# Performance work log

Hardware: AMD Instinct MI355X
Metric: run time of the kernel (lower is better)

## Reference

```python
import jax, jax.numpy as jnp
import numpy as np

B, S, DIM = 4, 512, 2048
E, INTER = 32, 1024
G, TOPK_G, TOPK = 8, 4, 6
ROUTE_SCALE = 2.5
SHARED_INTER = 2 * INTER  # n_shared_experts * moe_inter_dim


def setup_inputs() -> dict:
    key = jax.random.key(0)
    ks = jax.random.split(key, 8)
    sd = 0.02
    return {
        "x": jax.random.normal(ks[0], (B, S, DIM), jnp.float32),
        "gate_w": jax.random.normal(ks[1], (E, DIM), jnp.float32) * sd,
        "w11": jax.random.normal(ks[2], (E, INTER, DIM), jnp.float32) * sd,  # gate proj (torch Linear weight [out,in])
        "w33": jax.random.normal(ks[3], (E, INTER, DIM), jnp.float32) * sd,  # up proj
        "w22": jax.random.normal(ks[4], (E, DIM, INTER), jnp.float32) * sd,  # down proj
        "sw1": jax.random.normal(ks[5], (SHARED_INTER, DIM), jnp.float32) * sd,
        "sw2": jax.random.normal(ks[6], (DIM, SHARED_INTER), jnp.float32) * sd,
        "sw3": jax.random.normal(ks[7], (SHARED_INTER, DIM), jnp.float32) * sd,
    }


def _gate(xf, gate_w):
    # sigmoid scores, group-limited greedy top-k (bias=None branch)
    scores = jax.nn.sigmoid(xf @ gate_w.T)                      # [T, E]
    gs = scores.reshape(-1, G, E // G)                          # [T, G, E/G]
    group_scores = gs.max(axis=-1)                              # amax since bias is None
    _, gidx = jax.lax.top_k(group_scores, TOPK_G)               # [T, TOPK_G]
    gmask = jnp.any(jnp.arange(G)[None, None, :] == gidx[:, :, None], axis=1)  # [T, G] keep-mask
    masked = jnp.where(gmask[:, :, None], gs, -jnp.inf).reshape(-1, E)
    _, idx = jax.lax.top_k(masked, TOPK)                        # [T, TOPK]
    w = jnp.take_along_axis(scores, idx, axis=1)                # gather from original (pre-mask) scores
    w = w / jnp.sum(w, axis=-1, keepdims=True) * ROUTE_SCALE    # sigmoid normalization + route_scale
    return w, idx


def reference(x, gate_w, w11, w33, w22, sw1, sw2, sw3):
    xf = x.reshape(-1, DIM)                                     # [T, D]
    T = xf.shape[0]
    w, idx = _gate(xf, gate_w)
    # dense combine weights: equals the gather->gmm->scatter*prob of the original
    c = jnp.zeros((T, E), xf.dtype).at[jnp.arange(T)[:, None], idx].add(w)  # [T, E]
    g = jnp.einsum('td,eid->tei', xf, w11)                      # fc1 (gate)
    u = jnp.einsum('td,eid->tei', xf, w33)                      # fc2 (up)
    act = jax.nn.silu(g) * u                                    # fused SiLU gating
    y = jnp.einsum('tei,te,edi->td', act, c, w22)               # down proj + weighted combine
    shared = (jax.nn.silu(xf @ sw1.T) * (xf @ sw3.T)) @ sw2.T   # shared experts MLP
    return (y + shared).reshape(x.shape)
```

## Files before the change

### kernel.cpp

```cpp
#include <hip/hip_runtime.h>
#include <hip/hip_bf16.h>

#define T_TOK  2048
#define DIMSZ  2048
#define NEXP   32
#define INTERS 1024
#define SINTER 2048
#define NTOPK  6

typedef __bf16 bf16x8 __attribute__((ext_vector_type(8)));
typedef float  f32x4  __attribute__((ext_vector_type(4)));
typedef unsigned short u16x8 __attribute__((ext_vector_type(8)));

__device__ __forceinline__ unsigned short f2b(float f) {
    __hip_bfloat16 h = __float2bfloat16(f);
    return __builtin_bit_cast(unsigned short, h);
}

__device__ __forceinline__ void gl_lds16(const unsigned short* g, unsigned short* l) {
    __builtin_amdgcn_global_load_lds(
        (const __attribute__((address_space(1))) void*)g,
        (__attribute__((address_space(3))) void*)l, 16, 0, 0);
}

__device__ __forceinline__ void stage_b_f32(
    const float* __restrict__ B, int n0, int K, int k0,
    unsigned short* __restrict__ Bs, int tid)
{
    const int srow  = tid >> 3;
    const int s     = tid & 7;
    const int wslot = s ^ (srow & 7);
    #pragma unroll
    for (int p = 0; p < 4; ++p) {
        const int row = p * 32 + srow;
        const float* g = B + (size_t)(n0 + row) * K + k0 + s * 8;
        float4 a = *(const float4*)g;
        float4 b = *(const float4*)(g + 4);
        u16x8 o;
        o[0] = f2b(a.x); o[1] = f2b(a.y); o[2] = f2b(a.z); o[3] = f2b(a.w);
        o[4] = f2b(b.x); o[5] = f2b(b.y); o[6] = f2b(b.z); o[7] = f2b(b.w);
        *(u16x8*)&Bs[row * 64 + wslot * 8] = o;
    }
}

__global__ void cvt_f2b(const float4* __restrict__ src, unsigned short* __restrict__ dst, int n8) {
    int stride = gridDim.x * blockDim.x;
    for (int i = blockIdx.x * blockDim.x + threadIdx.x; i < n8; i += stride) {
        float4 a = src[2 * (size_t)i];
        float4 b = src[2 * (size_t)i + 1];
        u16x8 o;
        o[0] = f2b(a.x); o[1] = f2b(a.y); o[2] = f2b(a.z); o[3] = f2b(a.w);
        o[4] = f2b(b.x); o[5] = f2b(b.y); o[6] = f2b(b.z); o[7] = f2b(b.w);
        *(u16x8*)&dst[(size_t)i * 8] = o;
    }
}

#define SCT 8
#define SCK 128
__global__ __launch_bounds__(256) void gate_scores_kernel(
    const float* __restrict__ x, const float* __restrict__ gw, float* __restrict__ scores)
{
    __shared__ float xs[SCT * SCK];
    __shared__ float gs[NEXP * (SCK + 1)];
    const int t0 = blockIdx.x * SCT;
    const int tid = threadIdx.x;
    const int tl = tid >> 5, e = tid & 31;
    float acc = 0.f;
    for (int k0 = 0; k0 < DIMSZ; k0 += SCK) {
        {
            int row = tid >> 5, d4 = tid & 31;
            *(float4*)&xs[row * SCK + d4 * 4] =
                *(const float4*)&x[(size_t)(t0 + row) * DIMSZ + k0 + d4 * 4];
        }
        #pragma unroll
        for (int i = 0; i < 4; ++i) {
            int lin = tid + i * 256;
            int row = lin >> 5, d4 = lin & 31;
            float4 v = *(const float4*)&gw[(size_t)row * DIMSZ + k0 + d4 * 4];
            float* dst = &gs[row * (SCK + 1) + d4 * 4];
            dst[0] = v.x; dst[1] = v.y; dst[2] = v.z; dst[3] = v.w;
        }
        __syncthreads();
        #pragma unroll 8
        for (int d = 0; d < SCK; ++d)
            acc += xs[tl * SCK + d] * gs[e * (SCK + 1) + d];
        __syncthreads();
    }
    scores[(size_t)(t0 + tl) * NEXP + e] = 1.f / (1.f + expf(-acc));
}

__global__ __launch_bounds__(256) void topk_kernel(
    const float* __restrict__ scores,
    int* __restrict__ counts, int* __restrict__ toklist, float* __restrict__ wgts)
{
    int t = blockIdx.x * 256 + threadIdx.x;
    if (t >= T_TOK) return;
    float sc[NEXP];
    #pragma unroll
    for (int e = 0; e < NEXP; ++e) sc[e] = scores[(size_t)t * NEXP + e];

    float gsc[8];
    #pragma unroll
    for (int g = 0; g < 8; ++g) {
        float m = sc[4 * g];
        #pragma unroll
        for (int j = 1; j < 4; ++j) m = fmaxf(m, sc[4 * g + j]);
        gsc[g] = m;
    }
    bool gsel[8] = {false, false, false, false, false, false, false, false};
    for (int it = 0; it < 4; ++it) {
        int bi = -1; float bv = -1e30f;
        #pragma unroll
        for (int g = 0; g < 8; ++g)
            if (!gsel[g] && gsc[g] > bv) { bv = gsc[g]; bi = g; }
        gsel[bi] = true;
    }
    bool esel[NEXP];
    #pragma unroll
    for (int e = 0; e < NEXP; ++e) esel[e] = false;
    int   idx[NTOPK];
    float w[NTOPK];
    float sum = 0.f;
    for (int it = 0; it < NTOPK; ++it) {
        int bi = -1; float bv = -1e30f;
        #pragma unroll
        for (int e = 0; e < NEXP; ++e) {
            if (!gsel[e >> 2] || esel[e]) continue;
            if (sc[e] > bv) { bv = sc[e]; bi = e; }
        }
        esel[bi] = true; idx[it] = bi; w[it] = bv; sum += bv;
    }
    float scale = 2.5f / sum;
    for (int k = 0; k < NTOPK; ++k) {
        int e = idx[k];
        int s = atomicAdd(&counts[e], 1);
        toklist[e * T_TOK + s] = (t << 3) | k;
        wgts[e * T_TOK + s]   = w[k] * scale;
    }
}

__global__ __launch_bounds__(256, 2) void fc1_all(
    const unsigned short* __restrict__ A,
    const float* __restrict__ w11, const float* __restrict__ w33,
    const float* __restrict__ sw1, const float* __restrict__ sw3,
    unsigned short* __restrict__ h, unsigned short* __restrict__ hs,
    const int* __restrict__ counts, const int* __restrict__ toklist)
{
    constexpr int BM = 128, BN = 128, BK = 64, LDK = 64, K = DIMSZ;
    __shared__ unsigned short As[BM * LDK];
    __shared__ unsigned short B1s[BN * LDK];
    __shared__ unsigned short B2s[BN * LDK];
    __shared__ int aRowS[BM];
    __shared__ int cRowS[BM];
    __shared__ int map[4];

    const int tid = threadIdx.x;
    if (tid == 0) {
        const int wgid = blockIdx.x;
        if (wgid < 256) {
            map[0] = 1; map[1] = NEXP; map[2] = wgid >> 4; map[3] = wgid & 15;
        } else {
            const int rid = wgid - 256;
            const int xt = rid & 7, ty = rid >> 3;
            int acc2 = 0, fe = -1, fy = 0;
            #pragma unroll
            for (int e2 = 0; e2 < NEXP; ++e2) {
                const int nt = (counts[e2] + 127) >> 7;
                if (fe < 0 && ty < acc2 + nt) { fe = e2; fy = ty - acc2; }
                acc2 += nt;
            }
            map[0] = 0; map[1] = fe; map[2] = fy; map[3] = xt;
        }
    }
    __syncthreads();
    const bool SH = (map[0] != 0);
    const int e  = map[1];
    if (!SH && e < 0) return;
    const int m0 = map[2] * BM;
    const int n0 = map[3] * BN;
    const int N  = SH ? SINTER : INTERS;
    const int M  = SH ? T_TOK : counts[e];

    const size_t eoff = SH ? 0 : (size_t)e * INTERS * DIMSZ;
    const float* B1 = (SH ? sw1 : w11) + eoff;
    const float* B2 = (SH ? sw3 : w33) + eoff;
    unsigned short* Hout = SH ? hs : h;

    if (tid < BM) {
        int r = m0 + tid;
        if (SH) { aRowS[tid] = r; cRowS[tid] = r; }
        else if (r < M) {
            int ent = toklist[e * T_TOK + r];
            int t = ent >> 3, k = ent & 7;
            aRowS[tid] = t; cRowS[tid] = t * NTOPK + k;
        } else { aRowS[tid] = 0; cRowS[tid] = -1; }
    }
    __syncthreads();

    f32x4 acc1[4][4] = {};
    f32x4 acc2v[4][4] = {};

    const int wave = tid >> 6;
    const int lane = tid & 63;
    const int wm = (wave >> 1) * 64;
    const int wn = (wave & 1) * 64;
    const int lm = lane & 15;
    const int quad = lane >> 4;

    const unsigned short* aP[4];
    {
        const int l8 = lane >> 3;
        const int sg = (lane & 7) ^ l8;
        #pragma unroll
        for (int i = 0; i < 4; ++i) {
            const int c = wave * 4 + i;
            const int r = c * 8 + l8;
            aP[i] = A + (size_t)aRowS[r] * K + sg * 8;
        }
    }

    for (int k0 = 0; k0 < K; k0 += BK) {
        #pragma unroll
        for (int i = 0; i < 4; ++i) {
            const int c = wave * 4 + i;
            gl_lds16(aP[i] + k0, &As[c * 512]);
        }
        stage_b_f32(B1, n0, K, k0, B1s, tid);
        stage_b_f32(B2, n0, K, k0, B2s, tid);
        __syncthreads();
        #pragma unroll
        for (int kh = 0; kh < 2; ++kh) {
            const int soff = (((kh << 2) | quad) ^ (lm & 7)) << 3;
            bf16x8 af[4], bf1[4], bf2[4];
            #pragma unroll
            for (int ti = 0; ti < 4; ++ti)
                af[ti] = *(const bf16x8*)&As[(wm + ti * 16 + lm) * LDK + soff];
            #pragma unroll
            for (int tj = 0; tj < 4; ++tj) {
                bf1[tj] = *(const bf16x8*)&B1s[(wn + tj * 16 + lm) * LDK + soff];
                bf2[tj] = *(const bf16x8*)&B2s[(wn + tj * 16 + lm) * LDK + soff];
            }
            #pragma unroll
            for (int ti = 0; ti < 4; ++ti)
                #pragma unroll
                for (int tj = 0; tj < 4; ++tj) {
                    acc1[ti][tj] = __builtin_amdgcn_mfma_f32_16x16x32_bf16(
                        af[ti], bf1[tj], acc1[ti][tj], 0, 0, 0);
                    acc2v[ti][tj] = __builtin_amdgcn_mfma_f32_16x16x32_bf16(
                        af[ti], bf2[tj], acc2v[ti][tj], 0, 0, 0);
                }
        }
        __syncthreads();
    }

    #pragma unroll
    for (int ti = 0; ti < 4; ++ti) {
        #pragma unroll
        for (int r = 0; r < 4; ++r) {
            int lrow = wm + ti * 16 + quad * 4 + r;
            int cr = cRowS[lrow];
            if (cr < 0) continue;
            #pragma unroll
            for (int tj = 0; tj < 4; ++tj) {
                int nn = n0 + wn + tj * 16 + lm;
                float g = acc1[ti][tj][r];
                float u = acc2v[ti][tj][r];
                float hv = g / (1.f + expf(-g)) * u;
                Hout[(size_t)cr * N + nn] = f2b(hv);
            }
        }
    }
}

template <int MODE>
__global__ __launch_bounds__(256, 2) void fc2_all(
    const unsigned short* __restrict__ h, const unsigned short* __restrict__ hs,
    const float* __restrict__ w22, const float* __restrict__ sw2,
    float* __restrict__ yexp, float* __restrict__ out,
    const int* __restrict__ counts, const int* __restrict__ toklist,
    const float* __restrict__ wgts)
{
    constexpr int BM = 128, BN = 128, BK = 64, LDK = 64;
    __shared__ unsigned short As[BM * LDK];
    __shared__ unsigned short Bs[BN * LDK];
    __shared__ int   aRowS[BM];
    __shared__ int   cRowS[BM];
    __shared__ float cWS[BM];
    __shared__ int   map[4];

    const int tid = threadIdx.x;
    if (tid == 0) {
        const int wgid = blockIdx.x;
        if (MODE == 1 || (MODE == 0 && wgid < 256)) {
            const int sid = (MODE == 1) ? wgid : wgid;
            map[0] = 1; map[1] = NEXP; map[2] = sid >> 4; map[3] = sid & 15;
        } else {
            const int rid = (MODE == 0) ? (wgid - 256) : wgid;
            const int xt = rid & 15, ty = rid >> 4;
            int acc2 = 0, fe = -1, fy = 0;
            #pragma unroll
            for (int e2 = 0; e2 < NEXP; ++e2) {
                const int nt = (counts[e2] + 127) >> 7;
                if (fe < 0 && ty < acc2 + nt) { fe = e2; fy = ty - acc2; }
                acc2 += nt;
            }
            map[0] = 0; map[1] = fe; map[2] = fy; map[3] = xt;
        }
    }
    __syncthreads();
    const bool SH = (map[0] != 0);
    const int e  = map[1];
    if (!SH && e < 0) return;
    const int m0 = map[2] * BM;
    const int n0 = map[3] * BN;
    const int K  = SH ? SINTER : INTERS;
    const int M  = SH ? T_TOK : counts[e];

    const unsigned short* Asrc = SH ? hs : h;
    const float* B = SH ? sw2 : (w22 + (size_t)e * DIMSZ * INTERS);
    float* C = SH ? out : ((MODE == 2) ? out : yexp);

    if (tid < BM) {
        int r = m0 + tid;
        if (SH) { aRowS[tid] = r; cRowS[tid] = r; cWS[tid] = 1.f; }
        else if (r < M) {
            int ent = toklist[e * T_TOK + r];
            int slot = (ent >> 3) * NTOPK + (ent & 7);
            aRowS[tid] = slot;
            cRowS[tid] = (MODE == 2) ? (ent >> 3) : slot;
            cWS[tid] = wgts[e * T_TOK + r];
        } else { aRowS[tid] = 0; cRowS[tid] = -1; cWS[tid] = 0.f; }
    }
    __syncthreads();

    f32x4 acc[4][4] = {};

    const int wave = tid >> 6;
    const int lane = tid & 63;
    const int wm = (wave >> 1) * 64;
    const int wn = (wave & 1) * 64;
    const int lm = lane & 15;
    const int quad = lane >> 4;

    const unsigned short* aP[4];
    {
        const int l8 = lane >> 3;
        const int sg = (lane & 7) ^ l8;
        #pragma unroll
        for (int i = 0; i < 4; ++i) {
            const int c = wave * 4 + i;
            const int r = c * 8 + l8;
            aP[i] = Asrc + (size_t)aRowS[r] * K + sg * 8;
        }
    }

    for (int k0 = 0; k0 < K; k0 += BK) {
        #pragma unroll
        for (int i = 0; i < 4; ++i) {
            const int c = wave * 4 + i;
            gl_lds16(aP[i] + k0, &As[c * 512]);
        }
        stage_b_f32(B, n0, K, k0, Bs, tid);
        __syncthreads();
        #pragma unroll
        for (int kh = 0; kh < 2; ++kh) {
            const int soff = (((kh << 2) | quad) ^ (lm & 7)) << 3;
            bf16x8 af[4], bfr[4];
            #pragma unroll
            for (int ti = 0; ti < 4; ++ti)
                af[ti] = *(const bf16x8*)&As[(wm + ti * 16 + lm) * LDK + soff];
            #pragma unroll
            for (int tj = 0; tj < 4; ++tj)
                bfr[tj] = *(const bf16x8*)&Bs[(wn + tj * 16 + lm) * LDK + soff];
            #pragma unroll
            for (int ti = 0; ti < 4; ++ti)
                #pragma unroll
                for (int tj = 0; tj < 4; ++tj)
                    acc[ti][tj] = __builtin_amdgcn_mfma_f32_16x16x32_bf16(
                        af[ti], bfr[tj], acc[ti][tj], 0, 0, 0);
        }
        __syncthreads();
    }

    #pragma unroll
    for (int ti = 0; ti < 4; ++ti) {
        #pragma unroll
        for (int r = 0; r < 4; ++r) {
            int lrow = wm + ti * 16 + quad * 4 + r;
            int cr = cRowS[lrow];
            if (cr < 0) continue;
            #pragma unroll
            for (int tj = 0; tj < 4; ++tj) {
                int nn = n0 + wn + tj * 16 + lm;
                float v = acc[ti][tj][r] * cWS[lrow];
                if (MODE == 2 && !SH)
                    atomicAdd(&C[(size_t)cr * DIMSZ + nn], v);
                else
                    C[(size_t)cr * DIMSZ + nn] = v;
            }
        }
    }
}

__global__ __launch_bounds__(256) void combine_kernel(
    const float4* __restrict__ yexp, float4* __restrict__ out, int n4)
{
    const int D4 = DIMSZ / 4;
    int stride = gridDim.x * blockDim.x;
    for (int i = blockIdx.x * blockDim.x + threadIdx.x; i < n4; i += stride) {
        int t = i / D4, d4 = i - t * D4;
        const float4* r = yexp + (size_t)t * NTOPK * D4 + d4;
        float4 a = out[i];
        #pragma unroll
        for (int k = 0; k < NTOPK; ++k) {
            float4 s = r[(size_t)k * D4];
            a.x += s.x; a.y += s.y; a.z += s.z; a.w += s.w;
        }
        out[i] = a;
    }
}

extern "C" void kernel_launch(void* const* d_in, const int* in_sizes, int n_in,
                              void* d_out, int out_size, void* d_ws, size_t ws_size,
                              hipStream_t stream)
{
    const float* x   = (const float*)d_in[0];
    const float* gw  = (const float*)d_in[1];
    const float* w11 = (const float*)d_in[2];
    const float* w33 = (const float*)d_in[3];
    const float* w22 = (const float*)d_in[4];
    const float* sw1 = (const float*)d_in[5];
    const float* sw2 = (const float*)d_in[6];
    const float* sw3 = (const float*)d_in[7];
    float* out = (float*)d_out;

    char* ws = (char*)d_ws;
    size_t off = 0;
    auto alloc = [&](size_t b) { void* p = ws + off; off = (off + b + 255) & ~(size_t)255; return p; };
    int*            counts  = (int*)alloc(NEXP * 4);
    int*            toklist = (int*)alloc((size_t)NEXP * T_TOK * 4);
    float*          wgts    = (float*)alloc((size_t)NEXP * T_TOK * 4);
    float*          scores  = (float*)alloc((size_t)T_TOK * NEXP * 4);
    unsigned short* xb      = (unsigned short*)alloc((size_t)T_TOK * DIMSZ * 2);
    unsigned short* h       = (unsigned short*)alloc((size_t)T_TOK * NTOPK * INTERS * 2);
    unsigned short* hs      = (unsigned short*)alloc((size_t)T_TOK * SINTER * 2);

    const size_t yBytes = (size_t)T_TOK * NTOPK * DIMSZ * 4;
    const bool DENSE = (off + yBytes + 256) <= ws_size;
    float* yexp = DENSE ? (float*)alloc(yBytes) : nullptr;

    hipMemsetAsync(counts, 0, NEXP * 4, stream);

    const int n4x = T_TOK * DIMSZ / 4;
    cvt_f2b<<<1024, 256, 0, stream>>>((const float4*)x, xb, T_TOK * DIMSZ / 8);

    gate_scores_kernel<<<T_TOK / SCT, 256, 0, stream>>>(x, gw, scores);
    topk_kernel<<<(T_TOK + 255) / 256, 256, 0, stream>>>(scores, counts, toklist, wgts);

    fc1_all<<<256 + 1024, 256, 0, stream>>>(
        xb, w11, w33, sw1, sw3, h, hs, counts, toklist);

    if (DENSE) {
        fc2_all<0><<<256 + 2048, 256, 0, stream>>>(
            h, hs, w22, sw2, yexp, out, counts, toklist, wgts);
        combine_kernel<<<2048, 256, 0, stream>>>((const float4*)yexp, (float4*)out, n4x);
    } else {
        fc2_all<1><<<256, 256, 0, stream>>>(
            h, hs, w22, sw2, nullptr, out, counts, toklist, wgts);
        fc2_all<2><<<2048, 256, 0, stream>>>(
            h, hs, w22, sw2, nullptr, out, counts, toklist, wgts);
    }
}
```

Measured before the change: 1.093 ms.

## Software-pipeline fc1/fc2 GEMM loads with double-buffered A tile and register-prefetched B

The K loop in both expert GEMM kernels now issues the next tile's global loads before the MFMA work on the current tile. A is double-buffered in LDS through global_load_lds, and the fp32 weights for B are prefetched into registers, then converted to bf16 and written to LDS at the start of the next iteration. This is meant to hide global memory latency behind compute. It costs extra LDS and more registers (32 or 64 floats held per thread), and fc2's launch bounds are raised to request 3 workgroups per CU, which may cause register spills.

```diff
diff --git a/kernel.cpp b/kernel.cpp
--- a/kernel.cpp
+++ b/kernel.cpp
@@ -23,23 +23,27 @@
         (__attribute__((address_space(3))) void*)l, 16, 0, 0);
 }
 
-__device__ __forceinline__ void stage_b_f32(
+__device__ __forceinline__ void load_b8(
     const float* __restrict__ B, int n0, int K, int k0,
-    unsigned short* __restrict__ Bs, int tid)
-{
-    const int srow  = tid >> 3;
-    const int s     = tid & 7;
-    const int wslot = s ^ (srow & 7);
+    int srow, int sct, float4* r)
+{
     #pragma unroll
     for (int p = 0; p < 4; ++p) {
-        const int row = p * 32 + srow;
-        const float* g = B + (size_t)(n0 + row) * K + k0 + s * 8;
-        float4 a = *(const float4*)g;
-        float4 b = *(const float4*)(g + 4);
+        const float* g = B + (size_t)(n0 + p * 32 + srow) * K + k0 + sct * 8;
+        r[2 * p]     = *(const float4*)g;
+        r[2 * p + 1] = *(const float4*)(g + 4);
+    }
+}
+__device__ __forceinline__ void write_b8(
+    unsigned short* __restrict__ Bs, int srow, int wslot, const float4* r)
+{
+    #pragma unroll
+    for (int p = 0; p < 4; ++p) {
+        float4 a = r[2 * p], b = r[2 * p + 1];
         u16x8 o;
         o[0] = f2b(a.x); o[1] = f2b(a.y); o[2] = f2b(a.z); o[3] = f2b(a.w);
         o[4] = f2b(b.x); o[5] = f2b(b.y); o[6] = f2b(b.z); o[7] = f2b(b.w);
-        *(u16x8*)&Bs[row * 64 + wslot * 8] = o;
+        *(u16x8*)&Bs[(p * 32 + srow) * 64 + wslot * 8] = o;
     }
 }
 
@@ -147,7 +151,8 @@
     const int* __restrict__ counts, const int* __restrict__ toklist)
 {
     constexpr int BM = 128, BN = 128, BK = 64, LDK = 64, K = DIMSZ;
-    __shared__ unsigned short As[BM * LDK];
+    constexpr int ATILE = BM * LDK;
+    __shared__ unsigned short As[2 * ATILE];
     __shared__ unsigned short B1s[BN * LDK];
     __shared__ unsigned short B2s[BN * LDK];
     __shared__ int aRowS[BM];
@@ -206,6 +211,9 @@
     const int wn = (wave & 1) * 64;
     const int lm = lane & 15;
     const int quad = lane >> 4;
+    const int srow = tid >> 3;
+    const int sct  = tid & 7;
+    const int wslot = sct ^ (srow & 7);
 
     const unsigned short* aP[4];
     {
@@ -219,22 +227,35 @@
         }
     }
 
+    float4 r1[8], r2[8];
+    load_b8(B1, n0, K, 0, srow, sct, r1);
+    load_b8(B2, n0, K, 0, srow, sct, r2);
+    #pragma unroll
+    for (int i = 0; i < 4; ++i)
+        gl_lds16(aP[i], &As[(wave * 4 + i) * 512]);
+
+    int buf = 0;
     for (int k0 = 0; k0 < K; k0 += BK) {
-        #pragma unroll
-        for (int i = 0; i < 4; ++i) {
-            const int c = wave * 4 + i;
-            gl_lds16(aP[i] + k0, &As[c * 512]);
-        }
-        stage_b_f32(B1, n0, K, k0, B1s, tid);
-        stage_b_f32(B2, n0, K, k0, B2s, tid);
+        write_b8(B1s, srow, wslot, r1);
+        write_b8(B2s, srow, wslot, r2);
         __syncthreads();
+
+        if (k0 + BK < K) {
+            #pragma unroll
+            for (int i = 0; i < 4; ++i)
+                gl_lds16(aP[i] + k0 + BK, &As[(buf ^ 1) * ATILE + (wave * 4 + i) * 512]);
+            load_b8(B1, n0, K, k0 + BK, srow, sct, r1);
+            load_b8(B2, n0, K, k0 + BK, srow, sct, r2);
+        }
+
+        const unsigned short* Ac = &As[buf * ATILE];
         #pragma unroll
         for (int kh = 0; kh < 2; ++kh) {
             const int soff = (((kh << 2) | quad) ^ (lm & 7)) << 3;
             bf16x8 af[4], bf1[4], bf2[4];
             #pragma unroll
             for (int ti = 0; ti < 4; ++ti)
-                af[ti] = *(const bf16x8*)&As[(wm + ti * 16 + lm) * LDK + soff];
+                af[ti] = *(const bf16x8*)&Ac[(wm + ti * 16 + lm) * LDK + soff];
             #pragma unroll
             for (int tj = 0; tj < 4; ++tj) {
                 bf1[tj] = *(const bf16x8*)&B1s[(wn + tj * 16 + lm) * LDK + soff];
@@ -251,6 +272,7 @@
                 }
         }
         __syncthreads();
+        buf ^= 1;
     }
 
     #pragma unroll
@@ -273,7 +295,7 @@
 }
 
 template <int MODE>
-__global__ __launch_bounds__(256, 2) void fc2_all(
+__global__ __launch_bounds__(256, 3) void fc2_all(
     const unsigned short* __restrict__ h, const unsigned short* __restrict__ hs,
     const float* __restrict__ w22, const float* __restrict__ sw2,
     float* __restrict__ yexp, float* __restrict__ out,
@@ -281,7 +303,8 @@
     const float* __restrict__ wgts)
 {
     constexpr int BM = 128, BN = 128, BK = 64, LDK = 64;
-    __shared__ unsigned short As[BM * LDK];
+    constexpr int ATILE = BM * LDK;
+    __shared__ unsigned short As[2 * ATILE];
     __shared__ unsigned short Bs[BN * LDK];
     __shared__ int   aRowS[BM];
     __shared__ int   cRowS[BM];
@@ -292,7 +315,7 @@
     if (tid == 0) {
         const int wgid = blockIdx.x;
         if (MODE == 1 || (MODE == 0 && wgid < 256)) {
-            const int sid = (MODE == 1) ? wgid : wgid;
+            const int sid = wgid;
             map[0] = 1; map[1] = NEXP; map[2] = sid >> 4; map[3] = sid & 15;
         } else {
             const int rid = (MODE == 0) ? (wgid - 256) : wgid;
@@ -341,6 +364,9 @@
     const int wn = (wave & 1) * 64;
     const int lm = lane & 15;
     const int quad = lane >> 4;
+    const int srow = tid >> 3;
+    const int sct  = tid & 7;
+    const int wslot = sct ^ (srow & 7);
 
     const unsigned short* aP[4];
     {
@@ -354,21 +380,32 @@
         }
     }
 
+    float4 rb[8];
+    load_b8(B, n0, K, 0, srow, sct, rb);
+    #pragma unroll
+    for (int i = 0; i < 4; ++i)
+        gl_lds16(aP[i], &As[(wave * 4 + i) * 512]);
+
+    int buf = 0;
     for (int k0 = 0; k0 < K; k0 += BK) {
-        #pragma unroll
-        for (int i = 0; i < 4; ++i) {
-            const int c = wave * 4 + i;
-            gl_lds16(aP[i] + k0, &As[c * 512]);
-        }
-        stage_b_f32(B, n0, K, k0, Bs, tid);
+        write_b8(Bs, srow, wslot, rb);
         __syncthreads();
+
+        if (k0 + BK < K) {
+            #pragma unroll
+            for (int i = 0; i < 4; ++i)
+                gl_lds16(aP[i] + k0 + BK, &As[(buf ^ 1) * ATILE + (wave * 4 + i) * 512]);
+            load_b8(B, n0, K, k0 + BK, srow, sct, rb);
+        }
+
+        const unsigned short* Ac = &As[buf * ATILE];
         #pragma unroll
         for (int kh = 0; kh < 2; ++kh) {
             const int soff = (((kh << 2) | quad) ^ (lm & 7)) << 3;
             bf16x8 af[4], bfr[4];
             #pragma unroll
             for (int ti = 0; ti < 4; ++ti)
-                af[ti] = *(const bf16x8*)&As[(wm + ti * 16 + lm) * LDK + soff];
+                af[ti] = *(const bf16x8*)&Ac[(wm + ti * 16 + lm) * LDK + soff];
             #pragma unroll
             for (int tj = 0; tj < 4; ++tj)
                 bfr[tj] = *(const bf16x8*)&Bs[(wn + tj * 16 + lm) * LDK + soff];
@@ -380,6 +417,7 @@
                         af[ti], bfr[tj], acc[ti][tj], 0, 0, 0);
         }
         __syncthreads();
+        buf ^= 1;
     }
 
     #pragma unroll
```

Result: slower. 1.266 ms (+15.8%).

## Load fp32 weights directly to LDS and convert to bf16 at fragment read

Applied to the files above, without the earlier changes.

Weight tiles in fc1 and fc2 are now staged with global_load_lds as raw fp32 into a swizzled LDS buffer, replacing register-staged loads with bf16 conversion before the LDS write. Conversion to bf16 moves to the point where each wave reads its MFMA fragment. Per-tile row maps held in shared memory are replaced by direct toklist reads in registers, removing the setup syncthreads, and fc2 launch bounds rise to 3 blocks per CU with an early exit for empty row tiles. The cost is doubled LDS footprint and read traffic for B, plus repeated conversion work, since each B element is converted by several waves.

```diff
diff --git a/kernel.cpp b/kernel.cpp
--- a/kernel.cpp
+++ b/kernel.cpp
@@ -22,25 +22,17 @@
         (const __attribute__((address_space(1))) void*)g,
         (__attribute__((address_space(3))) void*)l, 16, 0, 0);
 }
-
-__device__ __forceinline__ void stage_b_f32(
-    const float* __restrict__ B, int n0, int K, int k0,
-    unsigned short* __restrict__ Bs, int tid)
-{
-    const int srow  = tid >> 3;
-    const int s     = tid & 7;
-    const int wslot = s ^ (srow & 7);
-    #pragma unroll
-    for (int p = 0; p < 4; ++p) {
-        const int row = p * 32 + srow;
-        const float* g = B + (size_t)(n0 + row) * K + k0 + s * 8;
-        float4 a = *(const float4*)g;
-        float4 b = *(const float4*)(g + 4);
-        u16x8 o;
-        o[0] = f2b(a.x); o[1] = f2b(a.y); o[2] = f2b(a.z); o[3] = f2b(a.w);
-        o[4] = f2b(b.x); o[5] = f2b(b.y); o[6] = f2b(b.z); o[7] = f2b(b.w);
-        *(u16x8*)&Bs[row * 64 + wslot * 8] = o;
-    }
+__device__ __forceinline__ void gl_lds16f(const float* g, float* l) {
+    __builtin_amdgcn_global_load_lds(
+        (const __attribute__((address_space(1))) void*)g,
+        (__attribute__((address_space(3))) void*)l, 16, 0, 0);
+}
+
+__device__ __forceinline__ bf16x8 cvt8(float4 lo, float4 hi) {
+    u16x8 u;
+    u[0] = f2b(lo.x); u[1] = f2b(lo.y); u[2] = f2b(lo.z); u[3] = f2b(lo.w);
+    u[4] = f2b(hi.x); u[5] = f2b(hi.y); u[6] = f2b(hi.z); u[7] = f2b(hi.w);
+    return __builtin_bit_cast(bf16x8, u);
 }
 
 __global__ void cvt_f2b(const float4* __restrict__ src, unsigned short* __restrict__ dst, int n8) {
@@ -139,6 +131,27 @@
     }
 }
 
+__device__ __forceinline__ void decode_tile(
+    int wgid, int xt_bits, const int* __restrict__ counts,
+    bool& SH, int& e, int& m0, int& n0)
+{
+    if (wgid < 256) {
+        SH = true; e = NEXP; m0 = (wgid >> 4) * 128; n0 = (wgid & 15) * 128;
+        return;
+    }
+    const int rid = wgid - 256;
+    const int xmask = (1 << xt_bits) - 1;
+    const int xt = rid & xmask, ty = rid >> xt_bits;
+    int acc2 = 0, fe = -1, fy = 0;
+    #pragma unroll
+    for (int e2 = 0; e2 < NEXP; ++e2) {
+        const int nt = (counts[e2] + 127) >> 7;
+        if (fe < 0 && ty < acc2 + nt) { fe = e2; fy = ty - acc2; }
+        acc2 += nt;
+    }
+    SH = false; e = fe; m0 = fy * 128; n0 = xt * 128;
+}
+
 __global__ __launch_bounds__(256, 2) void fc1_all(
     const unsigned short* __restrict__ A,
     const float* __restrict__ w11, const float* __restrict__ w33,
@@ -148,57 +161,20 @@
 {
     constexpr int BM = 128, BN = 128, BK = 64, LDK = 64, K = DIMSZ;
     __shared__ unsigned short As[BM * LDK];
-    __shared__ unsigned short B1s[BN * LDK];
-    __shared__ unsigned short B2s[BN * LDK];
-    __shared__ int aRowS[BM];
-    __shared__ int cRowS[BM];
-    __shared__ int map[4];
+    __shared__ float B1s[BN * BK];
+    __shared__ float B2s[BN * BK];
 
     const int tid = threadIdx.x;
-    if (tid == 0) {
-        const int wgid = blockIdx.x;
-        if (wgid < 256) {
-            map[0] = 1; map[1] = NEXP; map[2] = wgid >> 4; map[3] = wgid & 15;
-        } else {
-            const int rid = wgid - 256;
-            const int xt = rid & 7, ty = rid >> 3;
-            int acc2 = 0, fe = -1, fy = 0;
-            #pragma unroll
-            for (int e2 = 0; e2 < NEXP; ++e2) {
-                const int nt = (counts[e2] + 127) >> 7;
-                if (fe < 0 && ty < acc2 + nt) { fe = e2; fy = ty - acc2; }
-                acc2 += nt;
-            }
-            map[0] = 0; map[1] = fe; map[2] = fy; map[3] = xt;
-        }
-    }
-    __syncthreads();
-    const bool SH = (map[0] != 0);
-    const int e  = map[1];
+    bool SH; int e, m0, n0;
+    decode_tile(blockIdx.x, 3, counts, SH, e, m0, n0);
     if (!SH && e < 0) return;
-    const int m0 = map[2] * BM;
-    const int n0 = map[3] * BN;
-    const int N  = SH ? SINTER : INTERS;
-    const int M  = SH ? T_TOK : counts[e];
+    const int N = SH ? SINTER : INTERS;
+    const int M = SH ? T_TOK : counts[e];
 
     const size_t eoff = SH ? 0 : (size_t)e * INTERS * DIMSZ;
-    const float* B1 = (SH ? sw1 : w11) + eoff;
-    const float* B2 = (SH ? sw3 : w33) + eoff;
+    const float* B1 = (SH ? sw1 : w11) + eoff + (size_t)n0 * K;
+    const float* B2 = (SH ? sw3 : w33) + eoff + (size_t)n0 * K;
     unsigned short* Hout = SH ? hs : h;
-
-    if (tid < BM) {
-        int r = m0 + tid;
-        if (SH) { aRowS[tid] = r; cRowS[tid] = r; }
-        else if (r < M) {
-            int ent = toklist[e * T_TOK + r];
-            int t = ent >> 3, k = ent & 7;
-            aRowS[tid] = t; cRowS[tid] = t * NTOPK + k;
-        } else { aRowS[tid] = 0; cRowS[tid] = -1; }
-    }
-    __syncthreads();
-
-    f32x4 acc1[4][4] = {};
-    f32x4 acc2v[4][4] = {};
 
     const int wave = tid >> 6;
     const int lane = tid & 63;
@@ -213,32 +189,58 @@
         const int sg = (lane & 7) ^ l8;
         #pragma unroll
         for (int i = 0; i < 4; ++i) {
-            const int c = wave * 4 + i;
-            const int r = c * 8 + l8;
-            aP[i] = A + (size_t)aRowS[r] * K + sg * 8;
-        }
-    }
+            const int r = (wave * 4 + i) * 8 + l8;
+            int gr = m0 + r;
+            int ar;
+            if (SH) ar = gr;
+            else ar = (gr < M) ? (toklist[e * T_TOK + gr] >> 3) : 0;
+            aP[i] = A + (size_t)ar * K + sg * 8;
+        }
+    }
+    int offB[8];
+    {
+        #pragma unroll
+        for (int i = 0; i < 8; ++i) {
+            const int c = wave * 8 + i;
+            const int row = 4 * c + (lane >> 4);
+            const int g = (lane & 15) ^ (row & 7);
+            offB[i] = row * K + g * 4;
+        }
+    }
+
+    f32x4 acc1[4][4] = {};
+    f32x4 acc2v[4][4] = {};
 
     for (int k0 = 0; k0 < K; k0 += BK) {
         #pragma unroll
-        for (int i = 0; i < 4; ++i) {
-            const int c = wave * 4 + i;
-            gl_lds16(aP[i] + k0, &As[c * 512]);
-        }
-        stage_b_f32(B1, n0, K, k0, B1s, tid);
-        stage_b_f32(B2, n0, K, k0, B2s, tid);
+        for (int i = 0; i < 4; ++i)
+            gl_lds16(aP[i] + k0, &As[(wave * 4 + i) * 512]);
+        #pragma unroll
+        for (int i = 0; i < 8; ++i) {
+            const int c = wave * 8 + i;
+            gl_lds16f(B1 + offB[i] + k0, &B1s[c * 256]);
+            gl_lds16f(B2 + offB[i] + k0, &B2s[c * 256]);
+        }
         __syncthreads();
         #pragma unroll
         for (int kh = 0; kh < 2; ++kh) {
-            const int soff = (((kh << 2) | quad) ^ (lm & 7)) << 3;
+            const int soffA = (((kh << 2) | quad) ^ (lm & 7)) << 3;
+            const int j0 = ((kh << 2) | quad) << 1;
+            const int s0 = j0 ^ (lm & 7);
+            const int s1 = (j0 | 1) ^ (lm & 7);
             bf16x8 af[4], bf1[4], bf2[4];
             #pragma unroll
             for (int ti = 0; ti < 4; ++ti)
-                af[ti] = *(const bf16x8*)&As[(wm + ti * 16 + lm) * LDK + soff];
+                af[ti] = *(const bf16x8*)&As[(wm + ti * 16 + lm) * LDK + soffA];
             #pragma unroll
             for (int tj = 0; tj < 4; ++tj) {
-                bf1[tj] = *(const bf16x8*)&B1s[(wn + tj * 16 + lm) * LDK + soff];
-                bf2[tj] = *(const bf16x8*)&B2s[(wn + tj * 16 + lm) * LDK + soff];
+                const int rB = (wn + tj * 16 + lm) * 64;
+                float4 lo1 = *(const float4*)&B1s[rB + s0 * 4];
+                float4 hi1 = *(const float4*)&B1s[rB + s1 * 4];
+                bf1[tj] = cvt8(lo1, hi1);
+                float4 lo2 = *(const float4*)&B2s[rB + s0 * 4];
+                float4 hi2 = *(const float4*)&B2s[rB + s1 * 4];
+                bf2[tj] = cvt8(lo2, hi2);
             }
             #pragma unroll
             for (int ti = 0; ti < 4; ++ti)
@@ -257,9 +259,15 @@
     for (int ti = 0; ti < 4; ++ti) {
         #pragma unroll
         for (int r = 0; r < 4; ++r) {
-            int lrow = wm + ti * 16 + quad * 4 + r;
-            int cr = cRowS[lrow];
-            if (cr < 0) continue;
+            const int lrow = wm + ti * 16 + quad * 4 + r;
+            const int grow = m0 + lrow;
+            int cr;
+            if (SH) cr = grow;
+            else {
+                if (grow >= M) continue;
+                int ent = toklist[e * T_TOK + grow];
+                cr = (ent >> 3) * NTOPK + (ent & 7);
+            }
             #pragma unroll
             for (int tj = 0; tj < 4; ++tj) {
                 int nn = n0 + wn + tj * 16 + lm;
@@ -273,7 +281,7 @@
 }
 
 template <int MODE>
-__global__ __launch_bounds__(256, 2) void fc2_all(
+__global__ __launch_bounds__(256, 3) void fc2_all(
     const unsigned short* __restrict__ h, const unsigned short* __restrict__ hs,
     const float* __restrict__ w22, const float* __restrict__ sw2,
     float* __restrict__ yexp, float* __restrict__ out,
@@ -282,58 +290,24 @@
 {
     constexpr int BM = 128, BN = 128, BK = 64, LDK = 64;
     __shared__ unsigned short As[BM * LDK];
-    __shared__ unsigned short Bs[BN * LDK];
-    __shared__ int   aRowS[BM];
-    __shared__ int   cRowS[BM];
-    __shared__ float cWS[BM];
-    __shared__ int   map[4];
+    __shared__ float Bs[BN * BK];
 
     const int tid = threadIdx.x;
-    if (tid == 0) {
-        const int wgid = blockIdx.x;
-        if (MODE == 1 || (MODE == 0 && wgid < 256)) {
-            const int sid = (MODE == 1) ? wgid : wgid;
-            map[0] = 1; map[1] = NEXP; map[2] = sid >> 4; map[3] = sid & 15;
-        } else {
-            const int rid = (MODE == 0) ? (wgid - 256) : wgid;
-            const int xt = rid & 15, ty = rid >> 4;
-            int acc2 = 0, fe = -1, fy = 0;
-            #pragma unroll
-            for (int e2 = 0; e2 < NEXP; ++e2) {
-                const int nt = (counts[e2] + 127) >> 7;
-                if (fe < 0 && ty < acc2 + nt) { fe = e2; fy = ty - acc2; }
-                acc2 += nt;
-            }
-            map[0] = 0; map[1] = fe; map[2] = fy; map[3] = xt;
-        }
-    }
-    __syncthreads();
-    const bool SH = (map[0] != 0);
-    const int e  = map[1];
+    bool SH; int e, m0, n0;
+    {
+        int wgid = blockIdx.x;
+        if (MODE == 1) { SH = true; e = NEXP; m0 = (wgid >> 4) * 128; n0 = (wgid & 15) * 128; }
+        else if (MODE == 2) { decode_tile(wgid + 256, 4, counts, SH, e, m0, n0); }
+        else decode_tile(wgid, 4, counts, SH, e, m0, n0);
+    }
     if (!SH && e < 0) return;
-    const int m0 = map[2] * BM;
-    const int n0 = map[3] * BN;
-    const int K  = SH ? SINTER : INTERS;
-    const int M  = SH ? T_TOK : counts[e];
+    const int K = SH ? SINTER : INTERS;
+    const int M = SH ? T_TOK : counts[e];
+    if (m0 >= M) return;
 
     const unsigned short* Asrc = SH ? hs : h;
-    const float* B = SH ? sw2 : (w22 + (size_t)e * DIMSZ * INTERS);
+    const float* B = (SH ? sw2 : (w22 + (size_t)e * DIMSZ * INTERS)) + (size_t)n0 * K;
     float* C = SH ? out : ((MODE == 2) ? out : yexp);
-
-    if (tid < BM) {
-        int r = m0 + tid;
-        if (SH) { aRowS[tid] = r; cRowS[tid] = r; cWS[tid] = 1.f; }
-        else if (r < M) {
-            int ent = toklist[e * T_TOK + r];
-            int slot = (ent >> 3) * NTOPK + (ent & 7);
-            aRowS[tid] = slot;
-            cRowS[tid] = (MODE == 2) ? (ent >> 3) : slot;
-            cWS[tid] = wgts[e * T_TOK + r];
-        } else { aRowS[tid] = 0; cRowS[tid] = -1; cWS[tid] = 0.f; }
-    }
-    __syncthreads();
-
-    f32x4 acc[4][4] = {};
 
     const int wave = tid >> 6;
     const int lane = tid & 63;
@@ -348,30 +322,57 @@
         const int sg = (lane & 7) ^ l8;
         #pragma unroll
         for (int i = 0; i < 4; ++i) {
-            const int c = wave * 4 + i;
-            const int r = c * 8 + l8;
-            aP[i] = Asrc + (size_t)aRowS[r] * K + sg * 8;
-        }
-    }
+            const int r = (wave * 4 + i) * 8 + l8;
+            int gr = m0 + r;
+            int ar;
+            if (SH) ar = gr;
+            else if (gr < M) {
+                int ent = toklist[e * T_TOK + gr];
+                ar = (ent >> 3) * NTOPK + (ent & 7);
+            } else ar = 0;
+            aP[i] = Asrc + (size_t)ar * K + sg * 8;
+        }
+    }
+    int offB[8];
+    {
+        #pragma unroll
+        for (int i = 0; i < 8; ++i) {
+            const int c = wave * 8 + i;
+            const int row = 4 * c + (lane >> 4);
+            const int g = (lane & 15) ^ (row & 7);
+            offB[i] = row * K + g * 4;
+        }
+    }
+
+    f32x4 acc[4][4] = {};
 
     for (int k0 = 0; k0 < K; k0 += BK) {
         #pragma unroll
-        for (int i = 0; i < 4; ++i) {
-            const int c = wave * 4 + i;
-            gl_lds16(aP[i] + k0, &As[c * 512]);
-        }
-        stage_b_f32(B, n0, K, k0, Bs, tid);
+        for (int i = 0; i < 4; ++i)
+            gl_lds16(aP[i] + k0, &As[(wave * 4 + i) * 512]);
+        #pragma unroll
+        for (int i = 0; i < 8; ++i) {
+            const int c = wave * 8 + i;
+            gl_lds16f(B + offB[i] + k0, &Bs[c * 256]);
+        }
         __syncthreads();
         #pragma unroll
         for (int kh = 0; kh < 2; ++kh) {
-            const int soff = (((kh << 2) | quad) ^ (lm & 7)) << 3;
+            const int soffA = (((kh << 2) | quad) ^ (lm & 7)) << 3;
+            const int j0 = ((kh << 2) | quad) << 1;
+            const int s0 = j0 ^ (lm & 7);
+            const int s1 = (j0 | 1) ^ (lm & 7);
             bf16x8 af[4], bfr[4];
             #pragma unroll
             for (int ti = 0; ti < 4; ++ti)
-                af[ti] = *(const bf16x8*)&As[(wm + ti * 16 + lm) * LDK + soff];
-            #pragma unroll
-            for (int tj = 0; tj < 4; ++tj)
-                bfr[tj] = *(const bf16x8*)&Bs[(wn + tj * 16 + lm) * LDK + soff];
+                af[ti] = *(const bf16x8*)&As[(wm + ti * 16 + lm) * LDK + soffA];
+            #pragma unroll
+            for (int tj = 0; tj < 4; ++tj) {
+                const int rB = (wn + tj * 16 + lm) * 64;
+                float4 lo = *(const float4*)&Bs[rB + s0 * 4];
+                float4 hi = *(const float4*)&Bs[rB + s1 * 4];
+                bfr[tj] = cvt8(lo, hi);
+            }
             #pragma unroll
             for (int ti = 0; ti < 4; ++ti)
                 #pragma unroll
@@ -386,13 +387,20 @@
     for (int ti = 0; ti < 4; ++ti) {
         #pragma unroll
         for (int r = 0; r < 4; ++r) {
-            int lrow = wm + ti * 16 + quad * 4 + r;
-            int cr = cRowS[lrow];
-            if (cr < 0) continue;
+            const int lrow = wm + ti * 16 + quad * 4 + r;
+            const int grow = m0 + lrow;
+            int cr; float cw;
+            if (SH) { cr = grow; cw = 1.f; }
+            else {
+                if (grow >= M) continue;
+                int ent = toklist[e * T_TOK + grow];
+                cr = (MODE == 2) ? (ent >> 3) : ((ent >> 3) * NTOPK + (ent & 7));
+                cw = wgts[e * T_TOK + grow];
+            }
             #pragma unroll
             for (int tj = 0; tj < 4; ++tj) {
                 int nn = n0 + wn + tj * 16 + lm;
-                float v = acc[ti][tj][r] * cWS[lrow];
+                float v = acc[ti][tj][r] * cw;
                 if (MODE == 2 && !SH)
                     atomicAdd(&C[(size_t)cr * DIMSZ + nn], v);
                 else
```

Result: no change. 1.102 ms (+0.8%).
